# Kernel tuning notes

Measured on AMD Instinct MI355X. Metric: run time of the kernel, lower is better.

## Reference

```python
import jax, jax.numpy as jnp
import numpy as np

D_MODEL = 2048
NUM_Q_HEADS = 32
NUM_KV_HEADS = 8
HEAD_DIM = D_MODEL // NUM_Q_HEADS  # 64
NUM_GROUPS = NUM_Q_HEADS // NUM_KV_HEADS  # 4


def setup_inputs() -> dict:
    key = jax.random.key(0)
    ks = jax.random.split(key, 9)
    s = 1.0 / np.sqrt(D_MODEL)
    x = jax.random.normal(ks[0], (2, 2048, D_MODEL), dtype=jnp.float32)
    Wq = jax.random.uniform(ks[1], (D_MODEL, NUM_Q_HEADS * HEAD_DIM), jnp.float32, -s, s)
    bq = jax.random.uniform(ks[2], (NUM_Q_HEADS * HEAD_DIM,), jnp.float32, -s, s)
    Wk = jax.random.uniform(ks[3], (D_MODEL, NUM_KV_HEADS * HEAD_DIM), jnp.float32, -s, s)
    bk = jax.random.uniform(ks[4], (NUM_KV_HEADS * HEAD_DIM,), jnp.float32, -s, s)
    Wv = jax.random.uniform(ks[5], (D_MODEL, NUM_KV_HEADS * HEAD_DIM), jnp.float32, -s, s)
    bv = jax.random.uniform(ks[6], (NUM_KV_HEADS * HEAD_DIM,), jnp.float32, -s, s)
    Wo = jax.random.uniform(ks[7], (D_MODEL, D_MODEL), jnp.float32, -s, s)
    bo = jax.random.uniform(ks[8], (D_MODEL,), jnp.float32, -s, s)
    return {"x": x, "Wq": Wq, "bq": bq, "Wk": Wk, "bk": bk,
            "Wv": Wv, "bv": bv, "Wo": Wo, "bo": bo}


def reference(x, Wq, bq, Wk, bk, Wv, bv, Wo, bo):
    B, T, C = x.shape
    Hkv, G, Dh = NUM_KV_HEADS, NUM_GROUPS, HEAD_DIM
    # projections
    q = (x @ Wq + bq).reshape(B, T, Hkv, G, Dh)   # group G query heads per kv head
    k = (x @ Wk + bk).reshape(B, T, Hkv, Dh)
    v = (x @ Wv + bv).reshape(B, T, Hkv, Dh)
    scale = 1.0 / np.sqrt(Dh).astype(np.float32)
    # scores: [B, Hkv, G, T, T] (kv head broadcast over its G query heads)
    scores = jnp.einsum('btkgd,bskd->bkgts', q, k) * scale
    attn = jax.nn.softmax(scores, axis=-1)
    out = jnp.einsum('bkgts,bskd->btkgd', attn, v).reshape(B, T, C)
    return out @ Wo + bo
```

## Files before the change

kernel.cpp:

```cpp
#include <hip/hip_runtime.h>
#include <cstdint>
#include <cstddef>
#include <math.h>

typedef uint16_t bf16;
typedef __attribute__((ext_vector_type(8))) __bf16 bf16x8;
typedef __attribute__((ext_vector_type(4))) float f32x4;
typedef __attribute__((ext_vector_type(16))) float f32x16;

#define MFMA16(a,b,c) __builtin_amdgcn_mfma_f32_16x16x32_bf16((a),(b),(c),0,0,0)
#define MFMA32(a,b,c) __builtin_amdgcn_mfma_f32_32x32x16_bf16((a),(b),(c),0,0,0)

__device__ __forceinline__ uint16_t f2bf(float f){
  uint32_t u = __float_as_uint(f);
  return (uint16_t)((u + 0x7fffu + ((u >> 16) & 1u)) >> 16);
}
__device__ __forceinline__ uint32_t pk2(float lo, float hi){
  return (uint32_t)f2bf(lo) | ((uint32_t)f2bf(hi) << 16);
}

__device__ __forceinline__ void gload_lds16(const void* g, void* l){
  __builtin_amdgcn_global_load_lds((const __attribute__((address_space(1))) void*)g,
                                   (__attribute__((address_space(3))) void*)l, 16, 0, 0);
}

__device__ __forceinline__ void transpose64(const float* __restrict__ in, bf16* __restrict__ out,
                                            int R, int C, int c0, int r0, float* tileRaw){
  float (*tile)[65] = reinterpret_cast<float(*)[65]>(tileRaw);
  int t = threadIdx.x;
  int fx = t & 15, fy = t >> 4;
  #pragma unroll
  for (int i = 0; i < 4; i++){
    int r = fy + i*16;
    float4 v = *reinterpret_cast<const float4*>(in + (size_t)(r0 + r)*C + c0 + fx*4);
    tile[r][fx*4+0] = v.x; tile[r][fx*4+1] = v.y;
    tile[r][fx*4+2] = v.z; tile[r][fx*4+3] = v.w;
  }
  __syncthreads();
  int gx = t & 7, gy = t >> 3;
  #pragma unroll
  for (int i = 0; i < 2; i++){
    int c = gy + i*32;
    int rr = gx*8;
    union { bf16 h[8]; uint4 u; } pk_;
    #pragma unroll
    for (int j = 0; j < 8; j++) pk_.h[j] = f2bf(tile[rr+j][c]);
    *reinterpret_cast<uint4*>(out + (size_t)(c0 + c)*R + r0 + rr) = pk_.u;
  }
}

__global__ void k_prep(const float* __restrict__ x, bf16* __restrict__ xb,
                       const float* __restrict__ Wq, bf16* __restrict__ WqT,
                       const float* __restrict__ Wk, bf16* __restrict__ WkT,
                       const float* __restrict__ Wv, bf16* __restrict__ WvT){
  __shared__ __align__(16) float tile[64*65];
  int b = blockIdx.x;
  if (b < 8192){
    int i = (b * 256 + threadIdx.x) * 4;
    float4 v = *reinterpret_cast<const float4*>(x + i);
    uint2 pkv = make_uint2(pk2(v.x, v.y), pk2(v.z, v.w));
    *reinterpret_cast<uint2*>(xb + i) = pkv;
  } else if (b < 9216){
    int idx = b - 8192;
    transpose64(Wq, WqT, 2048, 2048, (idx & 31)*64, (idx >> 5)*64, tile);
  } else if (b < 9472){
    int idx = b - 9216;
    transpose64(Wk, WkT, 2048, 512, (idx & 7)*64, (idx >> 3)*64, tile);
  } else {
    int idx = b - 9472;
    transpose64(Wv, WvT, 2048, 512, (idx & 7)*64, (idx >> 3)*64, tile);
  }
}

__device__ __forceinline__ void gemm256_core(
    const bf16* __restrict__ Abase, const bf16* __restrict__ Btbase,
    char* lds, f32x4 acc[8][4])
{
  const int tid = threadIdx.x;
  const int wid = tid >> 6, lane = tid & 63;
  const int wm = wid >> 2, wn = wid & 3;
  const int lr = lane & 15, lg = lane >> 4;
  const f32x4 vzero = {0.f, 0.f, 0.f, 0.f};
  #pragma unroll
  for (int m = 0; m < 8; m++)
    #pragma unroll
    for (int n = 0; n < 4; n++)
      acc[m][n] = vzero;

  int srcH[2];
  #pragma unroll
  for (int i = 0; i < 2; i++){
    int db = i*8192 + tid*16;
    int row = db >> 7, sp = (db >> 4) & 7, sl = sp ^ (row & 7);
    srcH[i] = row*2048 + sl*8;
  }
  const int dOf = wid*1024;

  int ksl[2];
  #pragma unroll
  for (int ks = 0; ks < 2; ks++) ksl[ks] = (((ks*4 + lg) ^ (lr & 7)) << 4);
  const int aB = wm*16384 + lr*128;
  const int bB = 32768 + (wn >> 1)*16384 + (wn & 1)*8192 + lr*128;

  const bf16* Ab1 = Abase + 128*2048;
  const bf16* Bb1 = Btbase + 128*2048;

  #define STG_HALF(dstOff, gsrc) do { \
    gload_lds16((gsrc) + srcH[0], lds + (dstOff) + dOf); \
    gload_lds16((gsrc) + srcH[1], lds + (dstOff) + 8192 + dOf); \
  } while(0)

  STG_HALF(0,     Abase);
  STG_HALF(16384, Ab1);
  STG_HALF(32768, Btbase);
  STG_HALF(49152, Bb1);
  STG_HALF(65536, Abase + 64);
  asm volatile("s_waitcnt vmcnt(2)" ::: "memory");
  __builtin_amdgcn_s_barrier();

  bf16x8 afr[4][2], bfr[4][2];
  for (int t = 0; t < 32; t++){
    const int bo = (t & 1) * 65536;
    const int nb = bo ^ 65536;

    #pragma unroll
    for (int am = 0; am < 4; am++)
      #pragma unroll
      for (int ks = 0; ks < 2; ks++)
        afr[am][ks] = *reinterpret_cast<const bf16x8*>(lds + bo + aB + am*2048 + ksl[ks]);
    #pragma unroll
    for (int bn = 0; bn < 2; bn++)
      #pragma unroll
      for (int ks = 0; ks < 2; ks++)
        bfr[bn][ks] = *reinterpret_cast<const bf16x8*>(lds + bo + bB + bn*2048 + ksl[ks]);
    if (t < 31){
      STG_HALF(nb + 16384, Ab1 + (t+1)*64);
      STG_HALF(nb + 32768, Btbase + (t+1)*64);
      STG_HALF(nb + 49152, Bb1 + (t+1)*64);
    }
    __builtin_amdgcn_s_barrier();
    asm volatile("s_waitcnt lgkmcnt(0)" ::: "memory");
    __builtin_amdgcn_sched_barrier(0);
    __builtin_amdgcn_s_setprio(1);
    #pragma unroll
    for (int am = 0; am < 4; am++)
      #pragma unroll
      for (int bn = 0; bn < 2; bn++)
        #pragma unroll
        for (int ks = 0; ks < 2; ks++)
          acc[am][bn] = MFMA16(afr[am][ks], bfr[bn][ks], acc[am][bn]);
    __builtin_amdgcn_s_setprio(0);
    __builtin_amdgcn_s_barrier();

    #pragma unroll
    for (int bn = 2; bn < 4; bn++)
      #pragma unroll
      for (int ks = 0; ks < 2; ks++)
        bfr[bn][ks] = *reinterpret_cast<const bf16x8*>(lds + bo + bB + bn*2048 + ksl[ks]);
    __builtin_amdgcn_s_barrier();
    asm volatile("s_waitcnt lgkmcnt(0)" ::: "memory");
    __builtin_amdgcn_sched_barrier(0);
    __builtin_amdgcn_s_setprio(1);
    #pragma unroll
    for (int am = 0; am < 4; am++)
      #pragma unroll
      for (int bn = 2; bn < 4; bn++)
        #pragma unroll
        for (int ks = 0; ks < 2; ks++)
          acc[am][bn] = MFMA16(afr[am][ks], bfr[bn][ks], acc[am][bn]);
    __builtin_amdgcn_s_setprio(0);
    __builtin_amdgcn_s_barrier();

    #pragma unroll
    for (int am = 0; am < 4; am++)
      #pragma unroll
      for (int ks = 0; ks < 2; ks++)
        afr[am][ks] = *reinterpret_cast<const bf16x8*>(lds + bo + aB + (am+4)*2048 + ksl[ks]);
    __builtin_amdgcn_s_barrier();
    asm volatile("s_waitcnt lgkmcnt(0)" ::: "memory");
    __builtin_amdgcn_sched_barrier(0);
    __builtin_amdgcn_s_setprio(1);
    #pragma unroll
    for (int am = 0; am < 4; am++)
      #pragma unroll
      for (int bn = 0; bn < 2; bn++)
        #pragma unroll
        for (int ks = 0; ks < 2; ks++)
          acc[am+4][bn] = MFMA16(afr[am][ks], bfr[bn][ks], acc[am+4][bn]);
    __builtin_amdgcn_s_setprio(0);
    __builtin_amdgcn_s_barrier();

    if (t < 30) STG_HALF(bo, Abase + (t+2)*64);
    __builtin_amdgcn_s_barrier();
    __builtin_amdgcn_s_setprio(1);
    #pragma unroll
    for (int am = 0; am < 4; am++)
      #pragma unroll
      for (int bn = 2; bn < 4; bn++)
        #pragma unroll
        for (int ks = 0; ks < 2; ks++)
          acc[am+4][bn] = MFMA16(afr[am][ks], bfr[bn][ks], acc[am+4][bn]);
    __builtin_amdgcn_s_setprio(0);
    if (t < 30)       asm volatile("s_waitcnt vmcnt(2)" ::: "memory");
    else if (t == 30) asm volatile("s_waitcnt vmcnt(0)" ::: "memory");
    __builtin_amdgcn_sched_barrier(0);
    __builtin_amdgcn_s_barrier();
  }
  #undef STG_HALF
}

__device__ __forceinline__ void gemm256x128_core(
    const bf16* __restrict__ Abase, const bf16* __restrict__ Btbase,
    char* lds, f32x4 acc[8][2])
{
  const int tid = threadIdx.x;
  const int wid = tid >> 6, lane = tid & 63;
  const int wm = wid >> 2, wn = wid & 3;
  const int lr = lane & 15, lg = lane >> 4;
  const f32x4 vzero = {0.f, 0.f, 0.f, 0.f};
  #pragma unroll
  for (int m = 0; m < 8; m++)
    #pragma unroll
    for (int n = 0; n < 2; n++)
      acc[m][n] = vzero;

  int srcA[4], srcB[2];
  #pragma unroll
  for (int i = 0; i < 4; i++){
    int db = i*8192 + tid*16;
    int row = db >> 7, sp = (db >> 4) & 7, sl = sp ^ (row & 7);
    srcA[i] = row*2048 + sl*8;
  }
  #pragma unroll
  for (int i = 0; i < 2; i++){
    int db = i*8192 + tid*16;
    int row = db >> 7, sp = (db >> 4) & 7, sl = sp ^ (row & 7);
    srcB[i] = row*2048 + sl*8;
  }
  const int dOf = wid*1024;

  int ksl[2];
  #pragma unroll
  for (int ks = 0; ks < 2; ks++) ksl[ks] = (((ks*4 + lg) ^ (lr & 7)) << 4);
  const int aB = wm*16384 + lr*128;
  const int bB = wn*4096 + lr*128;

  #define STG_A(bufOff, koff) do { \
    gload_lds16(Abase + (koff) + srcA[0], lds + (bufOff) + dOf); \
    gload_lds16(Abase + (koff) + srcA[1], lds + (bufOff) + 8192 + dOf); \
    gload_lds16(Abase + (koff) + srcA[2], lds + (bufOff) + 16384 + dOf); \
    gload_lds16(Abase + (koff) + srcA[3], lds + (bufOff) + 24576 + dOf); \
  } while(0)
  #define STG_B(bufOff, koff) do { \
    gload_lds16(Btbase + (koff) + srcB[0], lds + (bufOff) + dOf); \
    gload_lds16(Btbase + (koff) + srcB[1], lds + (bufOff) + 8192 + dOf); \
  } while(0)

  STG_B(98304, 0);
  STG_A(0, 0);
  STG_B(114688, 64);
  STG_A(32768, 64);
  asm volatile("s_waitcnt vmcnt(6)" ::: "memory");
  __builtin_amdgcn_s_barrier();

  bf16x8 afr[8], bfr[2];
  int aOff = 0;
  int bIdx = 0;
  for (int t = 0; t < 32; t++){
    const int bOff = 98304 + bIdx*16384;
    const int aStg = (aOff == 0) ? 65536 : aOff - 32768;
    const int bStg = 98304 + ((bIdx == 0) ? 2 : bIdx - 1)*16384;

    #pragma unroll
    for (int am = 0; am < 8; am++)
      afr[am] = *reinterpret_cast<const bf16x8*>(lds + aOff + aB + am*2048 + ksl[0]);
    #pragma unroll
    for (int bn = 0; bn < 2; bn++)
      bfr[bn] = *reinterpret_cast<const bf16x8*>(lds + bOff + bB + bn*2048 + ksl[0]);
    if (t < 30) STG_B(bStg, (t+2)*64);
    __builtin_amdgcn_s_barrier();
    asm volatile("s_waitcnt lgkmcnt(0)" ::: "memory");
    __builtin_amdgcn_sched_barrier(0);
    __builtin_amdgcn_s_setprio(1);
    #pragma unroll
    for (int am = 0; am < 8; am++)
      #pragma unroll
      for (int bn = 0; bn < 2; bn++)
        acc[am][bn] = MFMA16(afr[am], bfr[bn], acc[am][bn]);
    __builtin_amdgcn_s_setprio(0);
    __builtin_amdgcn_s_barrier();

    #pragma unroll
    for (int am = 0; am < 8; am++)
      afr[am] = *reinterpret_cast<const bf16x8*>(lds + aOff + aB + am*2048 + ksl[1]);
    #pragma unroll
    for (int bn = 0; bn < 2; bn++)
      bfr[bn] = *reinterpret_cast<const bf16x8*>(lds + bOff + bB + bn*2048 + ksl[1]);
    if (t < 30) STG_A(aStg, (t+2)*64);
    __builtin_amdgcn_s_barrier();
    asm volatile("s_waitcnt lgkmcnt(0)" ::: "memory");
    __builtin_amdgcn_sched_barrier(0);
    __builtin_amdgcn_s_setprio(1);
    #pragma unroll
    for (int am = 0; am < 8; am++)
      #pragma unroll
      for (int bn = 0; bn < 2; bn++)
        acc[am][bn] = MFMA16(afr[am], bfr[bn], acc[am][bn]);
    __builtin_amdgcn_s_setprio(0);
    if (t < 30)       asm volatile("s_waitcnt vmcnt(6)" ::: "memory");
    else if (t == 30) asm volatile("s_waitcnt vmcnt(0)" ::: "memory");
    __builtin_amdgcn_sched_barrier(0);
    __builtin_amdgcn_s_barrier();

    aOff = (aOff == 65536) ? 0 : aOff + 32768;
    bIdx = (bIdx == 2) ? 0 : bIdx + 1;
  }
  #undef STG_A
  #undef STG_B
}

__global__ __launch_bounds__(512, 1) void k_qkv(
    const bf16* __restrict__ xb,
    const bf16* __restrict__ WqT, const bf16* __restrict__ WkT, const bf16* __restrict__ WvT,
    const float* __restrict__ bq, const float* __restrict__ bk, const float* __restrict__ bv,
    bf16* __restrict__ qo, bf16* __restrict__ ko, bf16* __restrict__ vtp,
    const float* __restrict__ Wo, bf16* __restrict__ WoT)
{
  __shared__ __align__(16) char lds[131072];
  int by = blockIdx.y;
  if (by >= 12){
    const int tb = (by - 12)*16 + blockIdx.x;
    const int half = threadIdx.x >> 8;
    const int t256 = threadIdx.x & 255;
    float (*tile)[65] = reinterpret_cast<float(*)[65]>(lds + half*16640);
    #pragma unroll 1
    for (int p = 0; p < 8; p++){
      int tIdx = tb*16 + p*2 + half;
      int c0 = (tIdx & 31)*64, r0 = (tIdx >> 5)*64;
      int fx = t256 & 15, fy = t256 >> 4;
      #pragma unroll
      for (int i = 0; i < 4; i++){
        int r = fy + i*16;
        float4 v = *reinterpret_cast<const float4*>(Wo + (size_t)(r0 + r)*2048 + c0 + fx*4);
        tile[r][fx*4+0] = v.x; tile[r][fx*4+1] = v.y;
        tile[r][fx*4+2] = v.z; tile[r][fx*4+3] = v.w;
      }
      __syncthreads();
      int gx = t256 & 7, gy = t256 >> 3;
      #pragma unroll
      for (int i = 0; i < 2; i++){
        int c = gy + i*32;
        int rr = gx*8;
        union { bf16 h[8]; uint4 u; } pk_;
        #pragma unroll
        for (int j = 0; j < 8; j++) pk_.h[j] = f2bf(tile[rr+j][c]);
        *reinterpret_cast<uint4*>(WoT + (size_t)(c0 + c)*2048 + r0 + rr) = pk_.u;
      }
      __syncthreads();
    }
    return;
  }
  const bf16* Bt; const float* bias; int mode; int y; float scale = 1.f;
  if (by < 8){       y = by;    Bt = WqT + (size_t)y*256*2048; bias = bq + y*256; mode = 0; scale = 0.18033688011112042f; }
  else if (by < 10){ y = by-8;  Bt = WkT + (size_t)y*256*2048; bias = bk + y*256; mode = 1; }
  else {             y = by-10; Bt = WvT + (size_t)y*256*2048; bias = bv + y*256; mode = 2; }
  int m0 = blockIdx.x * 256;
  f32x4 acc[8][4];
  gemm256_core(xb + (size_t)m0*2048, Bt, lds, acc);
  const int tid = threadIdx.x, wid = tid >> 6, lane = tid & 63;
  const int wm = wid >> 2, wn = wid & 3, lr = lane & 15, lg = lane >> 4;
  if (mode == 2){
    #pragma unroll
    for (int bn = 0; bn < 4; bn++){
      int c = wn*64 + bn*16 + lr;
      float bb = bias[c];
      int CL = y*256 + c;
      #pragma unroll
      for (int am = 0; am < 8; am++){
        int row0 = m0 + wm*128 + am*16 + lg*4;
        int bi = row0 >> 11, tl = row0 & 2047;
        union { bf16 h[4]; uint2 u; } pk_;
        #pragma unroll
        for (int r = 0; r < 4; r++) pk_.h[r] = f2bf(acc[am][bn][r] + bb);
        *reinterpret_cast<uint2*>(vtp + ((size_t)bi*512 + CL)*2048 + tl) = pk_.u;
      }
    }
  } else {
    bf16* outp = (mode == 0) ? (qo + y*256) : (ko + y*256);
    int ldc = (mode == 0) ? 2048 : 512;
    #pragma unroll
    for (int bn = 0; bn < 4; bn++){
      int c = wn*64 + bn*16 + lr;
      float bb = bias[c];
      #pragma unroll
      for (int am = 0; am < 8; am++)
        #pragma unroll
        for (int r = 0; r < 4; r++){
          int row = m0 + wm*128 + am*16 + lg*4 + r;
          outp[(size_t)row*ldc + c] = f2bf((acc[am][bn][r] + bb) * scale);
        }
    }
  }
}

__global__ __launch_bounds__(512, 1) void k_oproj(
    const bf16* __restrict__ ab, const bf16* __restrict__ WoT,
    const float* __restrict__ bo, float* __restrict__ outp)
{
  __shared__ __align__(16) char lds[147456];
  int m0 = blockIdx.x * 256, n0 = blockIdx.y * 128;
  f32x4 acc[8][2];
  gemm256x128_core(ab + (size_t)m0*2048, WoT + (size_t)n0*2048, lds, acc);
  const int tid = threadIdx.x, wid = tid >> 6, lane = tid & 63;
  const int wm = wid >> 2, wn = wid & 3, lr = lane & 15, lg = lane >> 4;
  #pragma unroll
  for (int bn = 0; bn < 2; bn++){
    int col = n0 + wn*32 + bn*16 + lr;
    float bb = bo[col];
    #pragma unroll
    for (int am = 0; am < 8; am++)
      #pragma unroll
      for (int r = 0; r < 4; r++){
        int row = m0 + wm*128 + am*16 + lg*4 + r;
        outp[(size_t)row*2048 + col] = acc[am][bn][r] + bb;
      }
  }
}

__global__ __launch_bounds__(512, 2) void k_flash(
    const bf16* __restrict__ q, const bf16* __restrict__ kmat,
    const bf16* __restrict__ vt, bf16* __restrict__ ao)
{
  __shared__ __align__(16) char lds[98304];
  const int tid = threadIdx.x;
  const int wid = tid >> 6, lane = tid & 63;
  const int l31 = lane & 31, hi = lane >> 5;
  const int bh = blockIdx.y;
  const int b = bh >> 5, hq = bh & 31, kvh = hq >> 2;
  const int qt = blockIdx.x;
  const int qrow0 = b*2048 + qt*512 + wid*64;

  bf16x8 qf[2][4];
  #pragma unroll
  for (int g = 0; g < 2; g++){
    const bf16* qrow = q + (size_t)(qrow0 + g*32 + l31)*2048 + hq*64 + hi*8;
    #pragma unroll
    for (int t = 0; t < 4; t++)
      qf[g][t] = *reinterpret_cast<const bf16x8*>(qrow + t*16);
  }

  f32x16 oacc[2][2];
  #pragma unroll
  for (int g = 0; g < 2; g++)
    #pragma unroll
    for (int n = 0; n < 2; n++)
      #pragma unroll
      for (int r = 0; r < 16; r++) oacc[g][n][r] = 0.f;
  float rsg[2][2];
  rsg[0][0]=0.f; rsg[0][1]=0.f; rsg[1][0]=0.f; rsg[1][1]=0.f;
  const f32x16 zv = {0.f,0.f,0.f,0.f,0.f,0.f,0.f,0.f,0.f,0.f,0.f,0.f,0.f,0.f,0.f,0.f};

  const int r7 = l31 & 7;
  int A[4];
  #pragma unroll
  for (int j = 0; j < 4; j++)
    A[j] = l31*128 + (((2*j + hi) ^ r7) << 4);

  const bf16* kbase = kmat + (size_t)b*2048*512 + kvh*64;
  const bf16* vbase = vt + ((size_t)b*512 + kvh*64)*2048;

  int kSrc[2], vSrc[2];
  const int dOf = wid*1024;
  #pragma unroll
  for (int i = 0; i < 2; i++){
    int kdb = i*8192 + tid*16;
    int krow = kdb >> 7, ksp = (kdb >> 4) & 7, ksl = ksp ^ (krow & 7);
    kSrc[i] = krow*512 + ksl*8;
    int o = tid*16;
    int vrow = o >> 7, vsp = (o >> 4) & 7, vsl = vsp ^ (vrow & 7);
    vSrc[i] = vrow*2048 + i*64 + vsl*8;
  }

  #define STAGE(bo, st_) do { \
    const bf16* kb_ = kbase + (size_t)(st_)*128*512; \
    const bf16* vb_ = vbase + (st_)*128; \
    gload_lds16(kb_ + kSrc[0], lds + (bo) + dOf); \
    gload_lds16(kb_ + kSrc[1], lds + (bo) + 8192 + dOf); \
    gload_lds16(vb_ + vSrc[0], lds + 49152 + (bo) + dOf); \
    gload_lds16(vb_ + vSrc[1], lds + 49152 + (bo) + 8192 + dOf); \
  } while(0)

  #define LDK(j, imm) (*reinterpret_cast<const bf16x8*>(lds + kOff + A[j] + (imm)))
  #define LDV(j, imm) (*reinterpret_cast<const bf16x8*>(lds + 49152 + kOff + A[j] + (imm)))

  STAGE(0, 0);
  STAGE(16384, 1);

  int kOff = 0;
  int sOff = 32768;
  for (int st = 0; st < 16; st++){
    if (st == 15) asm volatile("s_waitcnt vmcnt(0)" ::: "memory");
    else          asm volatile("s_waitcnt vmcnt(4)" ::: "memory");
    __builtin_amdgcn_sched_barrier(0);
    __builtin_amdgcn_s_barrier();
    __builtin_amdgcn_sched_barrier(0);
    if (st < 14){
      STAGE(sOff, st+2);
      sOff = (sOff == 32768) ? 0 : sOff + 16384;
    }

    #pragma unroll
    for (int c = 0; c < 2; c++){
      f32x16 sc[2][2];
      __builtin_amdgcn_s_setprio(1);
      #pragma unroll
      for (int t = 0; t < 4; t++){
        bf16x8 af0 = LDK(t, c*8192);
        bf16x8 af1 = LDK(t, c*8192 + 4096);
        if (t == 0){
          sc[0][0] = MFMA32(af0, qf[0][0], zv);
          sc[1][0] = MFMA32(af0, qf[1][0], zv);
          sc[0][1] = MFMA32(af1, qf[0][0], zv);
          sc[1][1] = MFMA32(af1, qf[1][0], zv);
        } else {
          sc[0][0] = MFMA32(af0, qf[0][t], sc[0][0]);
          sc[1][0] = MFMA32(af0, qf[1][t], sc[1][0]);
          sc[0][1] = MFMA32(af1, qf[0][t], sc[0][1]);
          sc[1][1] = MFMA32(af1, qf[1][t], sc[1][1]);
        }
      }
      __builtin_amdgcn_s_setprio(0);

      uint32_t pw[2][2][8];
      #pragma unroll
      for (int g = 0; g < 2; g++){
        #pragma unroll
        for (int n = 0; n < 2; n++)
          #pragma unroll
          for (int j = 0; j < 8; j++){
            float plo = __builtin_amdgcn_exp2f(sc[g][n][2*j]);
            float phi = __builtin_amdgcn_exp2f(sc[g][n][2*j+1]);
            rsg[g][j & 1] += plo + phi;
            asm("v_cvt_pk_bf16_f32 %0, %1, %2" : "=v"(pw[g][n][j]) : "v"(plo), "v"(phi));
          }
        #pragma unroll
        for (int n = 0; n < 2; n++)
          #pragma unroll
          for (int h = 0; h < 2; h++){
            asm volatile("v_permlane32_swap_b32 %0, %1" : "+v"(pw[g][n][h*4+0]), "+v"(pw[g][n][h*4+2]));
            asm volatile("v_permlane32_swap_b32 %0, %1" : "+v"(pw[g][n][h*4+1]), "+v"(pw[g][n][h*4+3]));
          }
      }

      __builtin_amdgcn_s_setprio(1);
      #pragma unroll
      for (int kk = 0; kk < 4; kk++){
        int n = kk >> 1, h = kk & 1;
        union { uint32_t w[4]; bf16x8 v; } pa0, pa1;
        #pragma unroll
        for (int w_ = 0; w_ < 4; w_++){ pa0.w[w_] = pw[0][n][h*4+w_]; pa1.w[w_] = pw[1][n][h*4+w_]; }
        #pragma unroll
        for (int nd = 0; nd < 2; nd++){
          bf16x8 vf = LDV(kk, c*8192 + nd*4096);
          oacc[0][nd] = MFMA32(pa0.v, vf, oacc[0][nd]);
          oacc[1][nd] = MFMA32(pa1.v, vf, oacc[1][nd]);
        }
      }
      __builtin_amdgcn_s_setprio(0);
    }
    kOff = (kOff == 32768) ? 0 : kOff + 16384;
  }
  #undef STAGE
  #undef LDK
  #undef LDV

  #pragma unroll
  for (int g = 0; g < 2; g++){
    float rs = rsg[g][0] + rsg[g][1];
    float l = rs + __shfl_xor(rs, 32);
    float linv = 1.f / l;
    float lv[16];
    #pragma unroll
    for (int r = 0; r < 16; r++){
      int qi = (r & 3) + 8*(r >> 2) + 4*hi;
      lv[r] = __shfl(linv, qi);
    }
    #pragma unroll
    for (int nd = 0; nd < 2; nd++)
      #pragma unroll
      for (int r = 0; r < 16; r++){
        int qi = (r & 3) + 8*(r >> 2) + 4*hi;
        int row = qrow0 + g*32 + qi;
        ao[(size_t)row*2048 + hq*64 + nd*32 + l31] = f2bf(oacc[g][nd][r] * lv[r]);
      }
  }
}

extern "C" void kernel_launch(void* const* d_in, const int* in_sizes, int n_in,
                              void* d_out, int out_size, void* d_ws, size_t ws_size,
                              hipStream_t stream)
{
  const float* x  = (const float*)d_in[0];
  const float* Wq = (const float*)d_in[1];
  const float* bq = (const float*)d_in[2];
  const float* Wk = (const float*)d_in[3];
  const float* bk = (const float*)d_in[4];
  const float* Wv = (const float*)d_in[5];
  const float* bv = (const float*)d_in[6];
  const float* Wo = (const float*)d_in[7];
  const float* bo = (const float*)d_in[8];
  float* out = (float*)d_out;

  char* ws = (char*)d_ws;
  size_t off = 0;
  auto alloc = [&](size_t bytes){ char* p = ws + off; off += (bytes + 255) & ~(size_t)255; return p; };
  bf16* xb  = (bf16*)alloc(2*2048*2048*2);
  bf16* WqT = (bf16*)alloc(2048*2048*2);
  bf16* WkT = (bf16*)alloc(512*2048*2);
  bf16* WvT = (bf16*)alloc(512*2048*2);
  bf16* WoT = (bf16*)alloc(2048*2048*2);
  bf16* qb  = (bf16*)alloc(4096*2048*2);
  bf16* kb  = (bf16*)alloc((size_t)4096*512*2);
  bf16* vtb = (bf16*)alloc((size_t)4096*512*2);
  bf16* aob = xb;

  k_prep<<<9728, 256, 0, stream>>>(x, xb, Wq, WqT, Wk, WkT, Wv, WvT);
  k_qkv<<<dim3(16,16), 512, 0, stream>>>(xb, WqT, WkT, WvT, bq, bk, bv, qb, kb, vtb, Wo, WoT);
  k_flash<<<dim3(4,64), 512, 0, stream>>>(qb, kb, vtb, aob);
  k_oproj<<<dim3(16,16), 512, 0, stream>>>(aob, WoT, bo, out);
}
```

Baseline: 189.6 us.

## Fuse QKV into one 256x192-tiled GEMM and move Wo transpose to prep

The QKV projection now treats the adjacent transposed Wq/Wk/Wv buffers as one concatenated weight. It uses a new 256x192 tile so all 256 blocks do equal GEMM work, with biases concatenated in a prep step. The Wo transpose, which used to run as extra blocks inside the QKV kernel, now runs in the prep kernel. The output-projection GEMM changes its wave layout from 2x4 waves of 128x32 to 4x2 waves of 64x64, which lowers LDS fragment reads per MFMA. The change relies on the three weight buffers being contiguous in the workspace, and it makes the prep kernel larger.

```diff
diff --git a/kernel.cpp b/kernel.cpp
--- a/kernel.cpp
+++ b/kernel.cpp
@@ -52,7 +52,10 @@
 __global__ void k_prep(const float* __restrict__ x, bf16* __restrict__ xb,
                        const float* __restrict__ Wq, bf16* __restrict__ WqT,
                        const float* __restrict__ Wk, bf16* __restrict__ WkT,
-                       const float* __restrict__ Wv, bf16* __restrict__ WvT){
+                       const float* __restrict__ Wv, bf16* __restrict__ WvT,
+                       const float* __restrict__ Wo, bf16* __restrict__ WoT,
+                       const float* __restrict__ bq, const float* __restrict__ bk,
+                       const float* __restrict__ bv, float* __restrict__ biasAll){
   __shared__ __align__(16) float tile[64*65];
   int b = blockIdx.x;
   if (b < 8192){
@@ -66,15 +69,25 @@
   } else if (b < 9472){
     int idx = b - 9216;
     transpose64(Wk, WkT, 2048, 512, (idx & 7)*64, (idx >> 3)*64, tile);
-  } else {
+  } else if (b < 9728){
     int idx = b - 9472;
     transpose64(Wv, WvT, 2048, 512, (idx & 7)*64, (idx >> 3)*64, tile);
-  }
-}
-
-__device__ __forceinline__ void gemm256_core(
+  } else if (b < 10752){
+    int idx = b - 9728;
+    transpose64(Wo, WoT, 2048, 2048, (idx & 31)*64, (idx >> 5)*64, tile);
+  } else {
+    int j = (b - 10752)*1024 + threadIdx.x*4;
+    float4 v;
+    if (j < 2048)      v = *reinterpret_cast<const float4*>(bq + j);
+    else if (j < 2560) v = *reinterpret_cast<const float4*>(bk + j - 2048);
+    else               v = *reinterpret_cast<const float4*>(bv + j - 2560);
+    *reinterpret_cast<float4*>(biasAll + j) = v;
+  }
+}
+
+__device__ __forceinline__ void gemm256x192_core(
     const bf16* __restrict__ Abase, const bf16* __restrict__ Btbase,
-    char* lds, f32x4 acc[8][4])
+    char* lds, f32x4 acc[8][3])
 {
   const int tid = threadIdx.x;
   const int wid = tid >> 6, lane = tid & 63;
@@ -84,147 +97,10 @@
   #pragma unroll
   for (int m = 0; m < 8; m++)
     #pragma unroll
-    for (int n = 0; n < 4; n++)
+    for (int n = 0; n < 3; n++)
       acc[m][n] = vzero;
 
-  int srcH[2];
-  #pragma unroll
-  for (int i = 0; i < 2; i++){
-    int db = i*8192 + tid*16;
-    int row = db >> 7, sp = (db >> 4) & 7, sl = sp ^ (row & 7);
-    srcH[i] = row*2048 + sl*8;
-  }
-  const int dOf = wid*1024;
-
-  int ksl[2];
-  #pragma unroll
-  for (int ks = 0; ks < 2; ks++) ksl[ks] = (((ks*4 + lg) ^ (lr & 7)) << 4);
-  const int aB = wm*16384 + lr*128;
-  const int bB = 32768 + (wn >> 1)*16384 + (wn & 1)*8192 + lr*128;
-
-  const bf16* Ab1 = Abase + 128*2048;
-  const bf16* Bb1 = Btbase + 128*2048;
-
-  #define STG_HALF(dstOff, gsrc) do { \
-    gload_lds16((gsrc) + srcH[0], lds + (dstOff) + dOf); \
-    gload_lds16((gsrc) + srcH[1], lds + (dstOff) + 8192 + dOf); \
-  } while(0)
-
-  STG_HALF(0,     Abase);
-  STG_HALF(16384, Ab1);
-  STG_HALF(32768, Btbase);
-  STG_HALF(49152, Bb1);
-  STG_HALF(65536, Abase + 64);
-  asm volatile("s_waitcnt vmcnt(2)" ::: "memory");
-  __builtin_amdgcn_s_barrier();
-
-  bf16x8 afr[4][2], bfr[4][2];
-  for (int t = 0; t < 32; t++){
-    const int bo = (t & 1) * 65536;
-    const int nb = bo ^ 65536;
-
-    #pragma unroll
-    for (int am = 0; am < 4; am++)
-      #pragma unroll
-      for (int ks = 0; ks < 2; ks++)
-        afr[am][ks] = *reinterpret_cast<const bf16x8*>(lds + bo + aB + am*2048 + ksl[ks]);
-    #pragma unroll
-    for (int bn = 0; bn < 2; bn++)
-      #pragma unroll
-      for (int ks = 0; ks < 2; ks++)
-        bfr[bn][ks] = *reinterpret_cast<const bf16x8*>(lds + bo + bB + bn*2048 + ksl[ks]);
-    if (t < 31){
-      STG_HALF(nb + 16384, Ab1 + (t+1)*64);
-      STG_HALF(nb + 32768, Btbase + (t+1)*64);
-      STG_HALF(nb + 49152, Bb1 + (t+1)*64);
-    }
-    __builtin_amdgcn_s_barrier();
-    asm volatile("s_waitcnt lgkmcnt(0)" ::: "memory");
-    __builtin_amdgcn_sched_barrier(0);
-    __builtin_amdgcn_s_setprio(1);
-    #pragma unroll
-    for (int am = 0; am < 4; am++)
-      #pragma unroll
-      for (int bn = 0; bn < 2; bn++)
-        #pragma unroll
-        for (int ks = 0; ks < 2; ks++)
-          acc[am][bn] = MFMA16(afr[am][ks], bfr[bn][ks], acc[am][bn]);
-    __builtin_amdgcn_s_setprio(0);
-    __builtin_amdgcn_s_barrier();
-
-    #pragma unroll
-    for (int bn = 2; bn < 4; bn++)
-      #pragma unroll
-      for (int ks = 0; ks < 2; ks++)
-        bfr[bn][ks] = *reinterpret_cast<const bf16x8*>(lds + bo + bB + bn*2048 + ksl[ks]);
-    __builtin_amdgcn_s_barrier();
-    asm volatile("s_waitcnt lgkmcnt(0)" ::: "memory");
-    __builtin_amdgcn_sched_barrier(0);
-    __builtin_amdgcn_s_setprio(1);
-    #pragma unroll
-    for (int am = 0; am < 4; am++)
-      #pragma unroll
-      for (int bn = 2; bn < 4; bn++)
-        #pragma unroll
-        for (int ks = 0; ks < 2; ks++)
-          acc[am][bn] = MFMA16(afr[am][ks], bfr[bn][ks], acc[am][bn]);
-    __builtin_amdgcn_s_setprio(0);
-    __builtin_amdgcn_s_barrier();
-
-    #pragma unroll
-    for (int am = 0; am < 4; am++)
-      #pragma unroll
-      for (int ks = 0; ks < 2; ks++)
-        afr[am][ks] = *reinterpret_cast<const bf16x8*>(lds + bo + aB + (am+4)*2048 + ksl[ks]);
-    __builtin_amdgcn_s_barrier();
-    asm volatile("s_waitcnt lgkmcnt(0)" ::: "memory");
-    __builtin_amdgcn_sched_barrier(0);
-    __builtin_amdgcn_s_setprio(1);
-    #pragma unroll
-    for (int am = 0; am < 4; am++)
-      #pragma unroll
-      for (int bn = 0; bn < 2; bn++)
-        #pragma unroll
-        for (int ks = 0; ks < 2; ks++)
-          acc[am+4][bn] = MFMA16(afr[am][ks], bfr[bn][ks], acc[am+4][bn]);
-    __builtin_amdgcn_s_setprio(0);
-    __builtin_amdgcn_s_barrier();
-
-    if (t < 30) STG_HALF(bo, Abase + (t+2)*64);
-    __builtin_amdgcn_s_barrier();
-    __builtin_amdgcn_s_setprio(1);
-    #pragma unroll
-    for (int am = 0; am < 4; am++)
-      #pragma unroll
-      for (int bn = 2; bn < 4; bn++)
-        #pragma unroll
-        for (int ks = 0; ks < 2; ks++)
-          acc[am+4][bn] = MFMA16(afr[am][ks], bfr[bn][ks], acc[am+4][bn]);
-    __builtin_amdgcn_s_setprio(0);
-    if (t < 30)       asm volatile("s_waitcnt vmcnt(2)" ::: "memory");
-    else if (t == 30) asm volatile("s_waitcnt vmcnt(0)" ::: "memory");
-    __builtin_amdgcn_sched_barrier(0);
-    __builtin_amdgcn_s_barrier();
-  }
-  #undef STG_HALF
-}
-
-__device__ __forceinline__ void gemm256x128_core(
-    const bf16* __restrict__ Abase, const bf16* __restrict__ Btbase,
-    char* lds, f32x4 acc[8][2])
-{
-  const int tid = threadIdx.x;
-  const int wid = tid >> 6, lane = tid & 63;
-  const int wm = wid >> 2, wn = wid & 3;
-  const int lr = lane & 15, lg = lane >> 4;
-  const f32x4 vzero = {0.f, 0.f, 0.f, 0.f};
-  #pragma unroll
-  for (int m = 0; m < 8; m++)
-    #pragma unroll
-    for (int n = 0; n < 2; n++)
-      acc[m][n] = vzero;
-
-  int srcA[4], srcB[2];
+  int srcA[4], srcB[3];
   #pragma unroll
   for (int i = 0; i < 4; i++){
     int db = i*8192 + tid*16;
@@ -232,6 +108,115 @@
     srcA[i] = row*2048 + sl*8;
   }
   #pragma unroll
+  for (int i = 0; i < 3; i++){
+    int db = i*8192 + tid*16;
+    int row = db >> 7, sp = (db >> 4) & 7, sl = sp ^ (row & 7);
+    srcB[i] = row*2048 + sl*8;
+  }
+  const int dOf = wid*1024;
+
+  int ksl[2];
+  #pragma unroll
+  for (int ks = 0; ks < 2; ks++) ksl[ks] = (((ks*4 + lg) ^ (lr & 7)) << 4);
+  const int aB = wm*16384 + lr*128;
+  const int bB = wn*6144 + lr*128;
+
+  #define STG_A(bufOff, koff) do { \
+    gload_lds16(Abase + (koff) + srcA[0], lds + (bufOff) + dOf); \
+    gload_lds16(Abase + (koff) + srcA[1], lds + (bufOff) + 8192 + dOf); \
+    gload_lds16(Abase + (koff) + srcA[2], lds + (bufOff) + 16384 + dOf); \
+    gload_lds16(Abase + (koff) + srcA[3], lds + (bufOff) + 24576 + dOf); \
+  } while(0)
+  #define STG_B(bufOff, koff) do { \
+    gload_lds16(Btbase + (koff) + srcB[0], lds + (bufOff) + dOf); \
+    gload_lds16(Btbase + (koff) + srcB[1], lds + (bufOff) + 8192 + dOf); \
+    gload_lds16(Btbase + (koff) + srcB[2], lds + (bufOff) + 16384 + dOf); \
+  } while(0)
+
+  STG_B(98304, 0);
+  STG_A(0, 0);
+  STG_A(32768, 64);
+  asm volatile("s_waitcnt vmcnt(4)" ::: "memory");
+  __builtin_amdgcn_s_barrier();
+
+  bf16x8 afr[8], bfr[3];
+  int aOff = 0;
+  int bOff = 98304;
+  for (int t = 0; t < 32; t++){
+    const int aStg = (aOff == 0) ? 65536 : aOff - 32768;
+    const int bNxt = bOff ^ 24576;
+
+    #pragma unroll
+    for (int am = 0; am < 8; am++)
+      afr[am] = *reinterpret_cast<const bf16x8*>(lds + aOff + aB + am*2048 + ksl[0]);
+    #pragma unroll
+    for (int bn = 0; bn < 3; bn++)
+      bfr[bn] = *reinterpret_cast<const bf16x8*>(lds + bOff + bB + bn*2048 + ksl[0]);
+    if (t < 31) STG_B(bNxt, (t+1)*64);
+    __builtin_amdgcn_s_barrier();
+    asm volatile("s_waitcnt lgkmcnt(0)" ::: "memory");
+    __builtin_amdgcn_sched_barrier(0);
+    __builtin_amdgcn_s_setprio(1);
+    #pragma unroll
+    for (int am = 0; am < 8; am++)
+      #pragma unroll
+      for (int bn = 0; bn < 3; bn++)
+        acc[am][bn] = MFMA16(afr[am], bfr[bn], acc[am][bn]);
+    __builtin_amdgcn_s_setprio(0);
+    __builtin_amdgcn_s_barrier();
+
+    #pragma unroll
+    for (int am = 0; am < 8; am++)
+      afr[am] = *reinterpret_cast<const bf16x8*>(lds + aOff + aB + am*2048 + ksl[1]);
+    #pragma unroll
+    for (int bn = 0; bn < 3; bn++)
+      bfr[bn] = *reinterpret_cast<const bf16x8*>(lds + bOff + bB + bn*2048 + ksl[1]);
+    if (t < 30) STG_A(aStg, (t+2)*64);
+    __builtin_amdgcn_s_barrier();
+    asm volatile("s_waitcnt lgkmcnt(0)" ::: "memory");
+    __builtin_amdgcn_sched_barrier(0);
+    __builtin_amdgcn_s_setprio(1);
+    #pragma unroll
+    for (int am = 0; am < 8; am++)
+      #pragma unroll
+      for (int bn = 0; bn < 3; bn++)
+        acc[am][bn] = MFMA16(afr[am], bfr[bn], acc[am][bn]);
+    __builtin_amdgcn_s_setprio(0);
+    if (t < 30)       asm volatile("s_waitcnt vmcnt(4)" ::: "memory");
+    else if (t == 30) asm volatile("s_waitcnt vmcnt(0)" ::: "memory");
+    __builtin_amdgcn_sched_barrier(0);
+    __builtin_amdgcn_s_barrier();
+
+    aOff = (aOff == 65536) ? 0 : aOff + 32768;
+    bOff = bNxt;
+  }
+  #undef STG_A
+  #undef STG_B
+}
+
+__device__ __forceinline__ void gemm256x128_core(
+    const bf16* __restrict__ Abase, const bf16* __restrict__ Btbase,
+    char* lds, f32x4 acc[4][4])
+{
+  const int tid = threadIdx.x;
+  const int wid = tid >> 6, lane = tid & 63;
+  const int wm = wid >> 1, wn = wid & 1;
+  const int lr = lane & 15, lg = lane >> 4;
+  const f32x4 vzero = {0.f, 0.f, 0.f, 0.f};
+  #pragma unroll
+  for (int m = 0; m < 4; m++)
+    #pragma unroll
+    for (int n = 0; n < 4; n++)
+      acc[m][n] = vzero;
+
+  int srcA[4], srcB[2];
+  #pragma unroll
+  for (int i = 0; i < 4; i++){
+    int db = i*8192 + tid*16;
+    int row = db >> 7, sp = (db >> 4) & 7, sl = sp ^ (row & 7);
+    srcA[i] = row*2048 + sl*8;
+  }
+  #pragma unroll
   for (int i = 0; i < 2; i++){
     int db = i*8192 + tid*16;
     int row = db >> 7, sp = (db >> 4) & 7, sl = sp ^ (row & 7);
@@ -242,8 +227,8 @@
   int ksl[2];
   #pragma unroll
   for (int ks = 0; ks < 2; ks++) ksl[ks] = (((ks*4 + lg) ^ (lr & 7)) << 4);
-  const int aB = wm*16384 + lr*128;
-  const int bB = wn*4096 + lr*128;
+  const int aB = wm*8192 + lr*128;
+  const int bB = wn*8192 + lr*128;
 
   #define STG_A(bufOff, koff) do { \
     gload_lds16(Abase + (koff) + srcA[0], lds + (bufOff) + dOf); \
@@ -263,7 +248,7 @@
   asm volatile("s_waitcnt vmcnt(6)" ::: "memory");
   __builtin_amdgcn_s_barrier();
 
-  bf16x8 afr[8], bfr[2];
+  bf16x8 afr[4], bfr[4];
   int aOff = 0;
   int bIdx = 0;
   for (int t = 0; t < 32; t++){
@@ -272,10 +257,10 @@
     const int bStg = 98304 + ((bIdx == 0) ? 2 : bIdx - 1)*16384;
 
     #pragma unroll
-    for (int am = 0; am < 8; am++)
+    for (int am = 0; am < 4; am++)
       afr[am] = *reinterpret_cast<const bf16x8*>(lds + aOff + aB + am*2048 + ksl[0]);
     #pragma unroll
-    for (int bn = 0; bn < 2; bn++)
+    for (int bn = 0; bn < 4; bn++)
       bfr[bn] = *reinterpret_cast<const bf16x8*>(lds + bOff + bB + bn*2048 + ksl[0]);
     if (t < 30) STG_B(bStg, (t+2)*64);
     __builtin_amdgcn_s_barrier();
@@ -283,18 +268,18 @@
     __builtin_amdgcn_sched_barrier(0);
     __builtin_amdgcn_s_setprio(1);
     #pragma unroll
-    for (int am = 0; am < 8; am++)
-      #pragma unroll
-      for (int bn = 0; bn < 2; bn++)
+    for (int am = 0; am < 4; am++)
+      #pragma unroll
+      for (int bn = 0; bn < 4; bn++)
         acc[am][bn] = MFMA16(afr[am], bfr[bn], acc[am][bn]);
     __builtin_amdgcn_s_setprio(0);
     __builtin_amdgcn_s_barrier();
 
     #pragma unroll
-    for (int am = 0; am < 8; am++)
+    for (int am = 0; am < 4; am++)
       afr[am] = *reinterpret_cast<const bf16x8*>(lds + aOff + aB + am*2048 + ksl[1]);
     #pragma unroll
-    for (int bn = 0; bn < 2; bn++)
+    for (int bn = 0; bn < 4; bn++)
       bfr[bn] = *reinterpret_cast<const bf16x8*>(lds + bOff + bB + bn*2048 + ksl[1]);
     if (t < 30) STG_A(aStg, (t+2)*64);
     __builtin_amdgcn_s_barrier();
@@ -302,9 +287,9 @@
     __builtin_amdgcn_sched_barrier(0);
     __builtin_amdgcn_s_setprio(1);
     #pragma unroll
-    for (int am = 0; am < 8; am++)
-      #pragma unroll
-      for (int bn = 0; bn < 2; bn++)
+    for (int am = 0; am < 4; am++)
+      #pragma unroll
+      for (int bn = 0; bn < 4; bn++)
         acc[am][bn] = MFMA16(afr[am], bfr[bn], acc[am][bn]);
     __builtin_amdgcn_s_setprio(0);
     if (t < 30)       asm volatile("s_waitcnt vmcnt(6)" ::: "memory");
@@ -320,61 +305,40 @@
 }
 
 __global__ __launch_bounds__(512, 1) void k_qkv(
-    const bf16* __restrict__ xb,
-    const bf16* __restrict__ WqT, const bf16* __restrict__ WkT, const bf16* __restrict__ WvT,
-    const float* __restrict__ bq, const float* __restrict__ bk, const float* __restrict__ bv,
-    bf16* __restrict__ qo, bf16* __restrict__ ko, bf16* __restrict__ vtp,
-    const float* __restrict__ Wo, bf16* __restrict__ WoT)
+    const bf16* __restrict__ xb, const bf16* __restrict__ WT,
+    const float* __restrict__ biasAll,
+    bf16* __restrict__ qo, bf16* __restrict__ ko, bf16* __restrict__ vtp)
 {
-  __shared__ __align__(16) char lds[131072];
-  int by = blockIdx.y;
-  if (by >= 12){
-    const int tb = (by - 12)*16 + blockIdx.x;
-    const int half = threadIdx.x >> 8;
-    const int t256 = threadIdx.x & 255;
-    float (*tile)[65] = reinterpret_cast<float(*)[65]>(lds + half*16640);
-    #pragma unroll 1
-    for (int p = 0; p < 8; p++){
-      int tIdx = tb*16 + p*2 + half;
-      int c0 = (tIdx & 31)*64, r0 = (tIdx >> 5)*64;
-      int fx = t256 & 15, fy = t256 >> 4;
-      #pragma unroll
-      for (int i = 0; i < 4; i++){
-        int r = fy + i*16;
-        float4 v = *reinterpret_cast<const float4*>(Wo + (size_t)(r0 + r)*2048 + c0 + fx*4);
-        tile[r][fx*4+0] = v.x; tile[r][fx*4+1] = v.y;
-        tile[r][fx*4+2] = v.z; tile[r][fx*4+3] = v.w;
-      }
-      __syncthreads();
-      int gx = t256 & 7, gy = t256 >> 3;
-      #pragma unroll
-      for (int i = 0; i < 2; i++){
-        int c = gy + i*32;
-        int rr = gx*8;
-        union { bf16 h[8]; uint4 u; } pk_;
-        #pragma unroll
-        for (int j = 0; j < 8; j++) pk_.h[j] = f2bf(tile[rr+j][c]);
-        *reinterpret_cast<uint4*>(WoT + (size_t)(c0 + c)*2048 + r0 + rr) = pk_.u;
-      }
-      __syncthreads();
-    }
-    return;
-  }
-  const bf16* Bt; const float* bias; int mode; int y; float scale = 1.f;
-  if (by < 8){       y = by;    Bt = WqT + (size_t)y*256*2048; bias = bq + y*256; mode = 0; scale = 0.18033688011112042f; }
-  else if (by < 10){ y = by-8;  Bt = WkT + (size_t)y*256*2048; bias = bk + y*256; mode = 1; }
-  else {             y = by-10; Bt = WvT + (size_t)y*256*2048; bias = bv + y*256; mode = 2; }
+  __shared__ __align__(16) char lds[147456];
   int m0 = blockIdx.x * 256;
-  f32x4 acc[8][4];
-  gemm256_core(xb + (size_t)m0*2048, Bt, lds, acc);
+  int y  = blockIdx.y;
+  f32x4 acc[8][3];
+  gemm256x192_core(xb + (size_t)m0*2048, WT + (size_t)y*192*2048, lds, acc);
   const int tid = threadIdx.x, wid = tid >> 6, lane = tid & 63;
   const int wm = wid >> 2, wn = wid & 3, lr = lane & 15, lg = lane >> 4;
-  if (mode == 2){
-    #pragma unroll
-    for (int bn = 0; bn < 4; bn++){
-      int c = wn*64 + bn*16 + lr;
-      float bb = bias[c];
-      int CL = y*256 + c;
+  #pragma unroll
+  for (int bn = 0; bn < 3; bn++){
+    int fb = y*192 + wn*48 + bn*16;
+    float bb = biasAll[fb + lr];
+    if (fb < 2048){
+      #pragma unroll
+      for (int am = 0; am < 8; am++)
+        #pragma unroll
+        for (int r = 0; r < 4; r++){
+          int row = m0 + wm*128 + am*16 + lg*4 + r;
+          qo[(size_t)row*2048 + fb + lr] = f2bf((acc[am][bn][r] + bb) * 0.18033688011112042f);
+        }
+    } else if (fb < 2560){
+      int c = fb - 2048 + lr;
+      #pragma unroll
+      for (int am = 0; am < 8; am++)
+        #pragma unroll
+        for (int r = 0; r < 4; r++){
+          int row = m0 + wm*128 + am*16 + lg*4 + r;
+          ko[(size_t)row*512 + c] = f2bf(acc[am][bn][r] + bb);
+        }
+    } else {
+      int vcol = fb - 2560 + lr;
       #pragma unroll
       for (int am = 0; am < 8; am++){
         int row0 = m0 + wm*128 + am*16 + lg*4;
@@ -382,23 +346,8 @@
         union { bf16 h[4]; uint2 u; } pk_;
         #pragma unroll
         for (int r = 0; r < 4; r++) pk_.h[r] = f2bf(acc[am][bn][r] + bb);
-        *reinterpret_cast<uint2*>(vtp + ((size_t)bi*512 + CL)*2048 + tl) = pk_.u;
+        *reinterpret_cast<uint2*>(vtp + ((size_t)bi*512 + vcol)*2048 + tl) = pk_.u;
       }
-    }
-  } else {
-    bf16* outp = (mode == 0) ? (qo + y*256) : (ko + y*256);
-    int ldc = (mode == 0) ? 2048 : 512;
-    #pragma unroll
-    for (int bn = 0; bn < 4; bn++){
-      int c = wn*64 + bn*16 + lr;
-      float bb = bias[c];
-      #pragma unroll
-      for (int am = 0; am < 8; am++)
-        #pragma unroll
-        for (int r = 0; r < 4; r++){
-          int row = m0 + wm*128 + am*16 + lg*4 + r;
-          outp[(size_t)row*ldc + c] = f2bf((acc[am][bn][r] + bb) * scale);
-        }
     }
   }
 }
@@ -409,19 +358,19 @@
 {
   __shared__ __align__(16) char lds[147456];
   int m0 = blockIdx.x * 256, n0 = blockIdx.y * 128;
-  f32x4 acc[8][2];
+  f32x4 acc[4][4];
   gemm256x128_core(ab + (size_t)m0*2048, WoT + (size_t)n0*2048, lds, acc);
   const int tid = threadIdx.x, wid = tid >> 6, lane = tid & 63;
-  const int wm = wid >> 2, wn = wid & 3, lr = lane & 15, lg = lane >> 4;
-  #pragma unroll
-  for (int bn = 0; bn < 2; bn++){
-    int col = n0 + wn*32 + bn*16 + lr;
+  const int wm = wid >> 1, wn = wid & 1, lr = lane & 15, lg = lane >> 4;
+  #pragma unroll
+  for (int bn = 0; bn < 4; bn++){
+    int col = n0 + wn*64 + bn*16 + lr;
     float bb = bo[col];
     #pragma unroll
-    for (int am = 0; am < 8; am++)
+    for (int am = 0; am < 4; am++)
       #pragma unroll
       for (int r = 0; r < 4; r++){
-        int row = m0 + wm*128 + am*16 + lg*4 + r;
+        int row = m0 + wm*64 + am*16 + lg*4 + r;
         outp[(size_t)row*2048 + col] = acc[am][bn][r] + bb;
       }
   }
@@ -622,10 +571,11 @@
   bf16* qb  = (bf16*)alloc(4096*2048*2);
   bf16* kb  = (bf16*)alloc((size_t)4096*512*2);
   bf16* vtb = (bf16*)alloc((size_t)4096*512*2);
+  float* biasAll = (float*)alloc(3072*4);
   bf16* aob = xb;
 
-  k_prep<<<9728, 256, 0, stream>>>(x, xb, Wq, WqT, Wk, WkT, Wv, WvT);
-  k_qkv<<<dim3(16,16), 512, 0, stream>>>(xb, WqT, WkT, WvT, bq, bk, bv, qb, kb, vtb, Wo, WoT);
+  k_prep<<<10755, 256, 0, stream>>>(x, xb, Wq, WqT, Wk, WkT, Wv, WvT, Wo, WoT, bq, bk, bv, biasAll);
+  k_qkv<<<dim3(16,16), 512, 0, stream>>>(xb, WqT, biasAll, qb, kb, vtb);
   k_flash<<<dim3(4,64), 512, 0, stream>>>(qb, kb, vtb, aob);
   k_oproj<<<dim3(16,16), 512, 0, stream>>>(aob, WoT, bo, out);
 }
```

New measurement: 181.7 us (median of 2 runs). 1.04x faster.
